# Kernel optimization log

Measured on AMD Instinct MI355X. Metric: run time of the kernel, lower is better.

Reference implementation:

```python
import jax, jax.numpy as jnp
import numpy as np

B, T, V, D, C = 64, 512, 100000, 256, 20
LN_EPS = 1e-5


def setup_inputs() -> dict:
    key = jax.random.key(0)
    ks = jax.random.split(key, 8)
    words = jax.random.randint(ks[0], (B, T), 0, V)
    seq_len = jax.random.randint(ks[1], (B,), 1, T + 1)  # at least 1 valid token
    target = jax.random.randint(ks[2], (B, T), 0, C)
    emb = jax.random.normal(ks[3], (V, D), jnp.float32) * 0.02
    ln_g = jnp.ones((D,), jnp.float32)
    ln_b = jnp.zeros((D,), jnp.float32)
    W = jax.random.normal(ks[4], (D, C), jnp.float32) * 0.05
    b = jnp.zeros((C,), jnp.float32)
    trans = jax.random.normal(ks[5], (C, C), jnp.float32) * 0.1
    start = jax.random.normal(ks[6], (C,), jnp.float32) * 0.1
    end = jax.random.normal(ks[7], (C,), jnp.float32) * 0.1
    return dict(words=words, seq_len=seq_len, target=target, emb=emb,
                ln_g=ln_g, ln_b=ln_b, W=W, b=b, trans=trans, start=start, end=end)


def _crf_nll(logits, tags, mask, trans, start, end):
    # logits: [B,T,C] log-softmax emissions; tags: [B,T] int; mask: [B,T] bool
    lt = jnp.transpose(logits, (1, 0, 2))  # [T,B,C]
    tt = jnp.transpose(tags)               # [T,B]
    mt = jnp.transpose(mask)               # [T,B]

    # ---- normalizer: forward algorithm (logsumexp recurrence) ----
    alpha0 = lt[0] + start[None, :]        # [B,C], include_start_end_trans

    def step(alpha, x):
        emit, m = x                        # emit: [B,C], m: [B]
        # [B, C_prev, C_next]
        scores = alpha[:, :, None] + trans[None, :, :] + emit[:, None, :]
        new = jax.scipy.special.logsumexp(scores, axis=1)
        return jnp.where(m[:, None], new, alpha), None

    alpha, _ = jax.lax.scan(step, alpha0, (lt[1:], mt[1:]))
    normalizer = jax.scipy.special.logsumexp(alpha + end[None, :], axis=-1)  # [B]

    # ---- gold score ----
    mf = mt.astype(logits.dtype)
    emit_sc = jnp.take_along_axis(lt, tt[:, :, None], axis=2)[:, :, 0]  # [T,B]
    emit_sum = jnp.sum(emit_sc * mf, axis=0)                            # [B]
    tr_sc = trans[tt[:-1], tt[1:]]                                      # [T-1,B]
    tr_sum = jnp.sum(tr_sc * mf[1:], axis=0)                            # [B]
    last = jnp.sum(mt.astype(jnp.int32), axis=0) - 1                    # [B]
    gold = emit_sum + tr_sum + start[tt[0]] + end[tt[last, jnp.arange(tt.shape[1])]]
    return normalizer - gold  # per-sequence NLL, [B]


def reference(words, seq_len, target, emb, ln_g, ln_b, W, b, trans, start, end):
    x = emb[words]                                      # [B,T,D] embedding gather
    mu = jnp.mean(x, axis=-1, keepdims=True)
    var = jnp.mean((x - mu) ** 2, axis=-1, keepdims=True)
    x = (x - mu) * jax.lax.rsqrt(var + LN_EPS) * ln_g + ln_b  # LayerNorm
    feats = x @ W + b                                   # [B,T,C]
    # dropout p=0.0 -> identity
    logits = jax.nn.log_softmax(feats, axis=-1)
    mask = jnp.arange(T)[None, :] < seq_len[:, None]    # seq_len_to_mask
    nll = _crf_nll(logits, target, mask, trans, start, end)
    return jnp.mean(nll)
```

## Files before the change

kernel.cpp:

```cpp
#include <hip/hip_runtime.h>
#include <math.h>

#define BB 64
#define TT 512
#define DD 256
#define CC 20
#define SS 32
#define LL 16
#define WW 16
#define PR 20
#define NSEG (BB * SS)
#define LN_EPS 1e-5f

__device__ __forceinline__ float dpp_sum16(float v) {
  v += __int_as_float(__builtin_amdgcn_update_dpp(0, __float_as_int(v), 0xB1, 0xF, 0xF, true));
  v += __int_as_float(__builtin_amdgcn_update_dpp(0, __float_as_int(v), 0x4E, 0xF, 0xF, true));
  v += __int_as_float(__builtin_amdgcn_update_dpp(0, __float_as_int(v), 0x141, 0xF, 0xF, true));
  v += __int_as_float(__builtin_amdgcn_update_dpp(0, __float_as_int(v), 0x140, 0xF, 0xF, true));
  return v;
}
__device__ __forceinline__ float dpp_max16(float v) {
  v = fmaxf(v, __int_as_float(__builtin_amdgcn_update_dpp(0, __float_as_int(v), 0xB1, 0xF, 0xF, true)));
  v = fmaxf(v, __int_as_float(__builtin_amdgcn_update_dpp(0, __float_as_int(v), 0x4E, 0xF, 0xF, true)));
  v = fmaxf(v, __int_as_float(__builtin_amdgcn_update_dpp(0, __float_as_int(v), 0x141, 0xF, 0xF, true)));
  v = fmaxf(v, __int_as_float(__builtin_amdgcn_update_dpp(0, __float_as_int(v), 0x140, 0xF, 0xF, true)));
  return v;
}
__device__ __forceinline__ float wave_reduce_sum64(float v) {
  #pragma unroll
  for (int off = 32; off > 0; off >>= 1) v += __shfl_xor(v, off, 64);
  return v;
}
__device__ __forceinline__ float wave_reduce_max64(float v) {
  #pragma unroll
  for (int off = 32; off > 0; off >>= 1) v = fmaxf(v, __shfl_xor(v, off, 64));
  return v;
}

__global__ __launch_bounds__(256, 1) void token_probs_kernel(
    const int* __restrict__ words, const float* __restrict__ emb,
    const float* __restrict__ ln_g, const float* __restrict__ ln_b,
    const float* __restrict__ W, const float* __restrict__ bias,
    float* __restrict__ probs)
{
  __shared__ __align__(16) float4 sW4[64 * 21];
  __shared__ float sb[CC];
  int tid = threadIdx.x;
  for (int ei = tid; ei < 64 * CC; ei += 256) {
    int d4 = ei / CC, c = ei - d4 * CC;
    int base = 4 * d4 * CC + c;
    sW4[d4 * 21 + c] = make_float4(W[base], W[base + CC], W[base + 2 * CC], W[base + 3 * CC]);
  }
  if (tid < CC) sb[tid] = bias[tid];
  __syncthreads();

  int l = tid & 15;
  int token = blockIdx.x * 16 + (tid >> 4);

  int word = words[token];
  const float4* row = (const float4*)(emb + (size_t)word * DD);
  float4 x0 = row[l], x1 = row[l + 16], x2 = row[l + 32], x3 = row[l + 48];

  float4 g0 = ((const float4*)ln_g)[l];
  float4 g1 = ((const float4*)ln_g)[l + 16];
  float4 g2 = ((const float4*)ln_g)[l + 32];
  float4 g3 = ((const float4*)ln_g)[l + 48];
  float4 e0v = ((const float4*)ln_b)[l];
  float4 e1v = ((const float4*)ln_b)[l + 16];
  float4 e2v = ((const float4*)ln_b)[l + 32];
  float4 e3v = ((const float4*)ln_b)[l + 48];

  float s1 = (x0.x + x0.y) + (x0.z + x0.w) + (x1.x + x1.y) + (x1.z + x1.w)
           + (x2.x + x2.y) + (x2.z + x2.w) + (x3.x + x3.y) + (x3.z + x3.w);
  float s2 = x0.x*x0.x + x0.y*x0.y + x0.z*x0.z + x0.w*x0.w
           + x1.x*x1.x + x1.y*x1.y + x1.z*x1.z + x1.w*x1.w
           + x2.x*x2.x + x2.y*x2.y + x2.z*x2.z + x2.w*x2.w
           + x3.x*x3.x + x3.y*x3.y + x3.z*x3.z + x3.w*x3.w;
  s1 = dpp_sum16(s1);
  s2 = dpp_sum16(s2);
  float mu = s1 * (1.f / DD);
  float var = s2 * (1.f / DD) - mu * mu;
  float rr = rsqrtf(var + LN_EPS);

  x0.x = (x0.x - mu) * rr * g0.x + e0v.x;  x0.y = (x0.y - mu) * rr * g0.y + e0v.y;
  x0.z = (x0.z - mu) * rr * g0.z + e0v.z;  x0.w = (x0.w - mu) * rr * g0.w + e0v.w;
  x1.x = (x1.x - mu) * rr * g1.x + e1v.x;  x1.y = (x1.y - mu) * rr * g1.y + e1v.y;
  x1.z = (x1.z - mu) * rr * g1.z + e1v.z;  x1.w = (x1.w - mu) * rr * g1.w + e1v.w;
  x2.x = (x2.x - mu) * rr * g2.x + e2v.x;  x2.y = (x2.y - mu) * rr * g2.y + e2v.y;
  x2.z = (x2.z - mu) * rr * g2.z + e2v.z;  x2.w = (x2.w - mu) * rr * g2.w + e2v.w;
  x3.x = (x3.x - mu) * rr * g3.x + e3v.x;  x3.y = (x3.y - mu) * rr * g3.y + e3v.y;
  x3.z = (x3.z - mu) * rr * g3.z + e3v.z;  x3.w = (x3.w - mu) * rr * g3.w + e3v.w;

  float f0 = 0.f, f1 = 0.f;
  #pragma unroll
  for (int c = 0; c < CC; ++c) {
    float4 w0 = sW4[l * 21 + c];
    float4 w1 = sW4[(l + 16) * 21 + c];
    float4 w2 = sW4[(l + 32) * 21 + c];
    float4 w3 = sW4[(l + 48) * 21 + c];
    float pp = (x0.x*w0.x + x0.y*w0.y) + (x0.z*w0.z + x0.w*w0.w)
             + (x1.x*w1.x + x1.y*w1.y) + (x1.z*w1.z + x1.w*w1.w)
             + (x2.x*w2.x + x2.y*w2.y) + (x2.z*w2.z + x2.w*w2.w)
             + (x3.x*w3.x + x3.y*w3.y) + (x3.z*w3.z + x3.w*w3.w);
    pp = dpp_sum16(pp) + sb[c];
    if (c < 16) { if (l == c) f0 = pp; }
    else        { if (l == c - 16) f1 = pp; }
  }

  float m = f0;
  if (l < 4) m = fmaxf(m, f1);
  m = dpp_max16(m);
  float q0 = __expf(f0 - m);
  float q1 = (l < 4) ? __expf(f1 - m) : 0.f;
  float ssum = dpp_sum16(q0 + q1);
  float inv = 1.0f / ssum;

  float* pt = probs + (size_t)token * PR;
  pt[l] = q0 * inv;
  if (l < 4) pt[16 + l] = q1 * inv;
}

__global__ __launch_bounds__(64, 1) void segment_kernel(
    const float* __restrict__ probs, const int* __restrict__ seq_len,
    const float* __restrict__ trans, const float* __restrict__ startv,
    float* __restrict__ partialZ, float* __restrict__ finalA)
{
  int tid = threadIdx.x;
  int grp = tid / 20;
  int l = tid - grp * 20;
  int chain = blockIdx.x * 3 + grp;
  bool act = (grp < 3) && (chain < NSEG);
  int ch = act ? chain : 0;
  int b = ch >> 5;
  int s = ch & (SS - 1);
  int len = seq_len[b];
  int base = act ? grp * 20 : 0;

  float E0  = __expf(trans[0*CC + l]),  E1  = __expf(trans[1*CC + l]);
  float E2  = __expf(trans[2*CC + l]),  E3  = __expf(trans[3*CC + l]);
  float E4  = __expf(trans[4*CC + l]),  E5  = __expf(trans[5*CC + l]);
  float E6  = __expf(trans[6*CC + l]),  E7  = __expf(trans[7*CC + l]);
  float E8  = __expf(trans[8*CC + l]),  E9  = __expf(trans[9*CC + l]);
  float E10 = __expf(trans[10*CC + l]), E11 = __expf(trans[11*CC + l]);
  float E12 = __expf(trans[12*CC + l]), E13 = __expf(trans[13*CC + l]);
  float E14 = __expf(trans[14*CC + l]), E15 = __expf(trans[15*CC + l]);
  float E16 = __expf(trans[16*CC + l]), E17 = __expf(trans[17*CC + l]);
  float E18 = __expf(trans[18*CC + l]), E19 = __expf(trans[19*CC + l]);

  int prod_start = s * LL + 1;
  int prod_end   = min(s * LL + LL, len - 1);
  bool empty = prod_start > prod_end;

  const float* pb = probs + (size_t)b * TT * PR + l;

  float v = (s == 0) ? pb[0] * __expf(startv[l]) : 1.0f;

#define STEP(t) do {                                            \
    float pr = pb[(t) * PR];                                    \
    float a0, a1, a2, a3;                                       \
    a0  = __shfl(v, base + 0, 64) * E0;                         \
    a1  = __shfl(v, base + 1, 64) * E1;                         \
    a2  = __shfl(v, base + 2, 64) * E2;                         \
    a3  = __shfl(v, base + 3, 64) * E3;                         \
    a0 += __shfl(v, base + 4, 64) * E4;                         \
    a1 += __shfl(v, base + 5, 64) * E5;                         \
    a2 += __shfl(v, base + 6, 64) * E6;                         \
    a3 += __shfl(v, base + 7, 64) * E7;                         \
    a0 += __shfl(v, base + 8, 64) * E8;                         \
    a1 += __shfl(v, base + 9, 64) * E9;                         \
    a2 += __shfl(v, base + 10, 64) * E10;                       \
    a3 += __shfl(v, base + 11, 64) * E11;                       \
    a0 += __shfl(v, base + 12, 64) * E12;                       \
    a1 += __shfl(v, base + 13, 64) * E13;                       \
    a2 += __shfl(v, base + 14, 64) * E14;                       \
    a3 += __shfl(v, base + 15, 64) * E15;                       \
    a0 += __shfl(v, base + 16, 64) * E16;                       \
    a1 += __shfl(v, base + 17, 64) * E17;                       \
    a2 += __shfl(v, base + 18, 64) * E18;                       \
    a3 += __shfl(v, base + 19, 64) * E19;                       \
    v = ((a0 + a1) + (a2 + a3)) * pr;                           \
  } while (0)

  int nwarm = (s == 0 || empty) ? 0 : WW;
  for (int t = prod_start - nwarm; t < prod_start; ++t) STEP(t);

  __shared__ float sv[64];
  sv[tid] = v;
  __syncthreads();
  float Smid = 0.f;
  #pragma unroll
  for (int i = 0; i < CC; ++i) Smid += sv[base + i];
  __syncthreads();

  if (!empty) {
    for (int t = prod_start; t <= prod_end; ++t) STEP(t);
  }
#undef STEP

  sv[tid] = v;
  __syncthreads();
  float Send = 0.f;
  #pragma unroll
  for (int i = 0; i < CC; ++i) Send += sv[base + i];

  if (act) {
    float pz;
    if (empty)       pz = 0.f;
    else if (s == 0) pz = __logf(Send);
    else             pz = __logf(Send) - __logf(Smid);
    if (l == 0) partialZ[ch] = pz;
    if (!empty && s == (len - 2) / LL)
      finalA[b * CC + l] = v / Send;
  }
}

__global__ __launch_bounds__(64, 1) void combine_kernel(
    const float* __restrict__ probs, const float* __restrict__ partialZ,
    const float* __restrict__ finalA, const int* __restrict__ seq_len,
    const int* __restrict__ target, const float* __restrict__ trans,
    const float* __restrict__ startv, const float* __restrict__ endv,
    float* __restrict__ out)
{
  int b = blockIdx.x;
  int j = threadIdx.x;
  int len = seq_len[b];
  const float* pb = probs + (size_t)b * TT * PR;
  const int* tg = target + b * TT;

  float gsum = 0.f;
  for (int t = j; t < len; t += 64) {
    int cur = tg[t];
    gsum += __logf(pb[(size_t)t * PR + cur]);
    if (t >= 1) gsum += trans[tg[t - 1] * CC + cur];
  }
  gsum = wave_reduce_sum64(gsum);

  float Z;
  if (len == 1) {
    float val = (j < CC) ? __logf(pb[j]) + startv[j] + endv[j] : -INFINITY;
    float m = wave_reduce_max64(val);
    float ssum = wave_reduce_sum64((j < CC) ? __expf(val - m) : 0.f);
    Z = m + __logf(ssum);
  } else {
    float pz = (j < SS) ? partialZ[b * SS + j] : 0.f;
    pz = wave_reduce_sum64(pz);
    float ve = (j < CC) ? finalA[b * CC + j] * __expf(endv[j]) : 0.f;
    float ssum = wave_reduce_sum64(ve);
    Z = pz + __logf(ssum);
  }

  if (j == 0) {
    float nll = Z - gsum - startv[tg[0]] - endv[tg[len - 1]];
    atomicAdd(out, nll * (1.0f / BB));
  }
}

extern "C" void kernel_launch(void* const* d_in, const int* in_sizes, int n_in,
                              void* d_out, int out_size, void* d_ws, size_t ws_size,
                              hipStream_t stream) {
  const int*   words   = (const int*)d_in[0];
  const int*   seq_len = (const int*)d_in[1];
  const int*   target  = (const int*)d_in[2];
  const float* emb     = (const float*)d_in[3];
  const float* ln_g    = (const float*)d_in[4];
  const float* ln_b    = (const float*)d_in[5];
  const float* W       = (const float*)d_in[6];
  const float* bias    = (const float*)d_in[7];
  const float* trans   = (const float*)d_in[8];
  const float* startv  = (const float*)d_in[9];
  const float* endv    = (const float*)d_in[10];

  float* probs    = (float*)d_ws;
  float* partialZ = probs + (size_t)BB * TT * PR;
  float* finalA   = partialZ + NSEG;
  float* out      = (float*)d_out;

  hipMemsetAsync(out, 0, sizeof(float), stream);
  token_probs_kernel<<<2048, 256, 0, stream>>>(words, emb, ln_g, ln_b, W, bias,
                                               probs);
  segment_kernel<<<(NSEG + 2) / 3, 64, 0, stream>>>(probs, seq_len, trans,
                                                    startv, partialZ, finalA);
  combine_kernel<<<BB, 64, 0, stream>>>(probs, partialZ, finalA, seq_len,
                                        target, trans, startv, endv, out);
}
```

Baseline: 184.8 us.

## Skip padded tokens, fuse gold-score into token kernel, replace atomic mean

The token kernel now exits early for blocks and threads past each sequence's length. It also computes the per-token gold emission, transition, start and end contributions directly from the logits, which removes the gather and log in the combine kernel. The segment kernel returns early for waves whose segments are all empty, and the final atomicAdd plus memset are replaced by a per-batch nll buffer and a small mean kernel. This adds an extra kernel launch and a goldEmit workspace write in exchange for skipping masked work.

```diff
diff --git a/kernel.cpp b/kernel.cpp
--- a/kernel.cpp
+++ b/kernel.cpp
@@ -41,8 +41,16 @@
     const int* __restrict__ words, const float* __restrict__ emb,
     const float* __restrict__ ln_g, const float* __restrict__ ln_b,
     const float* __restrict__ W, const float* __restrict__ bias,
-    float* __restrict__ probs)
+    const int* __restrict__ seq_len, const int* __restrict__ target,
+    const float* __restrict__ trans, const float* __restrict__ startv,
+    const float* __restrict__ endv,
+    float* __restrict__ probs, float* __restrict__ goldEmit)
 {
+  int b = blockIdx.x >> 5;
+  int t0 = (blockIdx.x & 31) << 4;
+  int len = seq_len[b];
+  if (t0 >= len) return;
+
   __shared__ __align__(16) float4 sW4[64 * 21];
   __shared__ float sb[CC];
   int tid = threadIdx.x;
@@ -55,7 +63,9 @@
   __syncthreads();
 
   int l = tid & 15;
-  int token = blockIdx.x * 16 + (tid >> 4);
+  int t = t0 + (tid >> 4);
+  if (t >= len) return;
+  int token = (b << 9) + t;
 
   int word = words[token];
   const float4* row = (const float4*)(emb + (size_t)word * DD);
@@ -91,7 +101,9 @@
   x3.x = (x3.x - mu) * rr * g3.x + e3v.x;  x3.y = (x3.y - mu) * rr * g3.y + e3v.y;
   x3.z = (x3.z - mu) * rr * g3.z + e3v.z;  x3.w = (x3.w - mu) * rr * g3.w + e3v.w;
 
+  int tgt = target[token];
   float f0 = 0.f, f1 = 0.f;
+  float ftgt = 0.f;
   #pragma unroll
   for (int c = 0; c < CC; ++c) {
     float4 w0 = sW4[l * 21 + c];
@@ -105,6 +117,8 @@
     pp = dpp_sum16(pp) + sb[c];
     if (c < 16) { if (l == c) f0 = pp; }
     else        { if (l == c - 16) f1 = pp; }
+    if (c < 16) { if (l == c && tgt == c) ftgt = pp; }
+    else        { if (l == c - 16 && tgt == c) ftgt = pp; }
   }
 
   float m = f0;
@@ -114,10 +128,20 @@
   float q1 = (l < 4) ? __expf(f1 - m) : 0.f;
   float ssum = dpp_sum16(q0 + q1);
   float inv = 1.0f / ssum;
+  float lsm = m + __logf(ssum);
+  ftgt = dpp_sum16(ftgt);
 
   float* pt = probs + (size_t)token * PR;
   pt[l] = q0 * inv;
   if (l < 4) pt[16 + l] = q1 * inv;
+
+  if (l == 0) {
+    float g = ftgt - lsm;
+    if (t > 0) g += trans[target[token - 1] * CC + tgt];
+    else       g += startv[tgt];
+    if (t == len - 1) g += endv[tgt];
+    goldEmit[token] = g;
+  }
 }
 
 __global__ __launch_bounds__(64, 1) void segment_kernel(
@@ -136,6 +160,15 @@
   int len = seq_len[b];
   int base = act ? grp * 20 : 0;
 
+  int prod_start = s * LL + 1;
+  int prod_end   = min(s * LL + LL, len - 1);
+  bool empty = prod_start > prod_end;
+
+  if (__ballot(act && !empty) == 0ull) {
+    if (act && l == 0) partialZ[ch] = 0.f;
+    return;
+  }
+
   float E0  = __expf(trans[0*CC + l]),  E1  = __expf(trans[1*CC + l]);
   float E2  = __expf(trans[2*CC + l]),  E3  = __expf(trans[3*CC + l]);
   float E4  = __expf(trans[4*CC + l]),  E5  = __expf(trans[5*CC + l]);
@@ -146,10 +179,6 @@
   float E14 = __expf(trans[14*CC + l]), E15 = __expf(trans[15*CC + l]);
   float E16 = __expf(trans[16*CC + l]), E17 = __expf(trans[17*CC + l]);
   float E18 = __expf(trans[18*CC + l]), E19 = __expf(trans[19*CC + l]);
-
-  int prod_start = s * LL + 1;
-  int prod_end   = min(s * LL + LL, len - 1);
-  bool empty = prod_start > prod_end;
 
   const float* pb = probs + (size_t)b * TT * PR + l;
 
@@ -216,27 +245,22 @@
 
 __global__ __launch_bounds__(64, 1) void combine_kernel(
     const float* __restrict__ probs, const float* __restrict__ partialZ,
-    const float* __restrict__ finalA, const int* __restrict__ seq_len,
-    const int* __restrict__ target, const float* __restrict__ trans,
-    const float* __restrict__ startv, const float* __restrict__ endv,
-    float* __restrict__ out)
+    const float* __restrict__ finalA, const float* __restrict__ goldEmit,
+    const int* __restrict__ seq_len, const float* __restrict__ startv,
+    const float* __restrict__ endv, float* __restrict__ nll)
 {
   int b = blockIdx.x;
   int j = threadIdx.x;
   int len = seq_len[b];
-  const float* pb = probs + (size_t)b * TT * PR;
-  const int* tg = target + b * TT;
 
   float gsum = 0.f;
-  for (int t = j; t < len; t += 64) {
-    int cur = tg[t];
-    gsum += __logf(pb[(size_t)t * PR + cur]);
-    if (t >= 1) gsum += trans[tg[t - 1] * CC + cur];
-  }
+  const float* ge = goldEmit + ((size_t)b << 9);
+  for (int t = j; t < len; t += 64) gsum += ge[t];
   gsum = wave_reduce_sum64(gsum);
 
   float Z;
   if (len == 1) {
+    const float* pb = probs + (size_t)b * TT * PR;
     float val = (j < CC) ? __logf(pb[j]) + startv[j] + endv[j] : -INFINITY;
     float m = wave_reduce_max64(val);
     float ssum = wave_reduce_sum64((j < CC) ? __expf(val - m) : 0.f);
@@ -249,10 +273,15 @@
     Z = pz + __logf(ssum);
   }
 
-  if (j == 0) {
-    float nll = Z - gsum - startv[tg[0]] - endv[tg[len - 1]];
-    atomicAdd(out, nll * (1.0f / BB));
-  }
+  if (j == 0) nll[b] = Z - gsum;
+}
+
+__global__ __launch_bounds__(64) void mean_kernel(
+    const float* __restrict__ nll, float* __restrict__ out)
+{
+  float v = nll[threadIdx.x];
+  v = wave_reduce_sum64(v);
+  if (threadIdx.x == 0) out[0] = v * (1.0f / BB);
 }
 
 extern "C" void kernel_launch(void* const* d_in, const int* in_sizes, int n_in,
@@ -271,15 +300,18 @@
   const float* endv    = (const float*)d_in[10];
 
   float* probs    = (float*)d_ws;
-  float* partialZ = probs + (size_t)BB * TT * PR;
+  float* goldEmit = probs + (size_t)BB * TT * PR;
+  float* partialZ = goldEmit + (size_t)BB * TT;
   float* finalA   = partialZ + NSEG;
+  float* nll      = finalA + BB * CC;
   float* out      = (float*)d_out;
 
-  hipMemsetAsync(out, 0, sizeof(float), stream);
   token_probs_kernel<<<2048, 256, 0, stream>>>(words, emb, ln_g, ln_b, W, bias,
-                                               probs);
+                                               seq_len, target, trans, startv,
+                                               endv, probs, goldEmit);
   segment_kernel<<<(NSEG + 2) / 3, 64, 0, stream>>>(probs, seq_len, trans,
                                                     startv, partialZ, finalA);
-  combine_kernel<<<BB, 64, 0, stream>>>(probs, partialZ, finalA, seq_len,
-                                        target, trans, startv, endv, out);
-}
+  combine_kernel<<<BB, 64, 0, stream>>>(probs, partialZ, finalA, goldEmit,
+                                        seq_len, startv, endv, nll);
+  mean_kernel<<<1, 64, 0, stream>>>(nll, out);
+}
```

Result: faster. 180.6 us (-2.2%).
